# Optimization experiments

Hardware: AMD Instinct MI355X
Metric: run time of the kernel (lower is better)

The kernel has to match this reference:

```python
import jax, jax.numpy as jnp
import numpy as np

B, H, L, D = 1, 8, 2048, 64
DP = 3   # positional coord dim
RE = 1   # extra relative features appended via concat
F = DP + RE  # LazyLinear in-features


def setup_inputs() -> dict:
    key = jax.random.key(0)
    ks = jax.random.split(key, 12)
    return {
        "q": jax.random.normal(ks[0], (B, H, L, D), jnp.float32),
        "k": jax.random.normal(ks[1], (B, H, L, D), jnp.float32),
        "v": jax.random.normal(ks[2], (B, H, L, D), jnp.float32),
        "c": jax.random.uniform(ks[3], (B, 1, 1, L), jnp.float32),
        "d_q": jax.random.normal(ks[4], (B, L, DP), jnp.float32),
        "d_k_top": jax.random.normal(ks[5], (B, L, DP), jnp.float32),
        "d_k_bot": jax.random.normal(ks[6], (B, L, DP), jnp.float32),
        "d_k_score": jax.random.uniform(ks[7], (B, L, 2, F), jnp.float32),
        "relative_top": jax.random.normal(ks[8], (B, L, L, RE), jnp.float32),
        "relative_bottom": jax.random.normal(ks[9], (B, L, L, RE), jnp.float32),
        "W_w": jax.random.normal(ks[10], (F, H), jnp.float32) * 0.1,
        "W_b": jax.random.normal(ks[11], (F, H), jnp.float32) * 0.1,
    }


def _pairwise_diff(a, b):
    # a: [B,Lq,Dp], b: [B,Lk,Dp] -> [B,Lq,Lk,Dp]
    return a[:, :, None, :] - b[:, None, :, :]


def reference(q, k, v, c, d_q, d_k_top, d_k_bot, d_k_score,
              relative_top, relative_bottom, W_w, W_b):
    # score function: scaled dot product -> [B,H,Lq,Lk]
    scores = jnp.einsum('bhqd,bhkd->bhqk', q, k) * (q.shape[-1] ** -0.5)

    # relative-position bias path
    dt = jnp.concatenate([_pairwise_diff(d_q, d_k_top), relative_top], axis=-1)     # [B,Lq,Lk,F]
    db = jnp.concatenate([_pairwise_diff(d_q, d_k_bot), relative_bottom], axis=-1)  # [B,Lq,Lk,F]
    dm = jnp.stack([dt, db], axis=3)                 # [B,Lq,Lk,2,F]
    dm = dm * d_k_score[:, None]                     # broadcast over Lq
    dm = dm.sum(axis=3)                              # [B,Lq,Lk,F]

    w = jax.nn.softplus(dm @ W_w).transpose(0, 3, 1, 2)  # [B,H,Lq,Lk]
    b = (dm @ W_b).transpose(0, 3, 1, 2)                 # [B,H,Lq,Lk]
    scores = scores * w + b

    # leaky probability function: softmax gated by per-key sampling weights c
    probs = jax.nn.softmax(scores, axis=-1) * c      # [B,H,Lq,Lk]

    out = jnp.einsum('bhqk,bhkd->bhqd', probs, v)
    return out, probs
```

## Files before the change

### kernel.cpp

```cpp
#include <hip/hip_runtime.h>
#include <cstdint>
#include <cstddef>

#define NH 8
#define LQ 2048
#define DH 64
#define NKT_HALF 16

typedef __attribute__((ext_vector_type(8))) __bf16 bf16x8;
typedef __attribute__((ext_vector_type(8))) unsigned short ushort8;
typedef __attribute__((ext_vector_type(4))) float floatx4;

__device__ __forceinline__ unsigned short bf_trunc(float x) {
    return (unsigned short)(__float_as_uint(x) >> 16);
}
__device__ __forceinline__ float bf_up(unsigned short h) {
    return __uint_as_float(((unsigned int)h) << 16);
}
__device__ __forceinline__ unsigned short bf_rne(float x) {
    unsigned int u = __float_as_uint(x);
    return (unsigned short)((u + 0x7FFFu + ((u >> 16) & 1u)) >> 16);
}
struct hl_t { unsigned short h, l; };
__device__ __forceinline__ hl_t split2(float x) {
    hl_t r;
    r.h = bf_trunc(x);
    r.l = bf_trunc(x - bf_up(r.h));
    return r;
}

#define MFMA16(A, B, C) __builtin_amdgcn_mfma_f32_16x16x32_bf16((A), (B), (C), 0, 0, 0)

__global__ __launch_bounds__(256, 3) void attn_main(
    const float* __restrict__ qp,  const float* __restrict__ kp,
    const float* __restrict__ vp,  const float* __restrict__ cp,
    const float* __restrict__ dqp, const float* __restrict__ dktp,
    const float* __restrict__ dkbp,const float* __restrict__ dksp,
    const float* __restrict__ rtp, const float* __restrict__ rbp,
    const float* __restrict__ Wwp, const float* __restrict__ Wbp,
    float* __restrict__ probp, float* __restrict__ lws, float* __restrict__ pvws)
{
    __shared__ unsigned short sh_khi[64 * 72];
    __shared__ unsigned short sh_klo[64 * 72];
    __shared__ unsigned short sh_vhi[64 * 72];
    __shared__ unsigned short sh_vlo[64 * 72];
    __shared__ float sh_meta[64 * 13];
    __shared__ float sh_dqs[64 * 3];

    const int bid  = blockIdx.x;
    const int half = bid & 1;
    const int h    = (bid >> 1) & 7;
    const int qt   = bid >> 4;
    const int q0   = qt * 64;
    const int t    = threadIdx.x;
    const int lane = t & 63;
    const int m    = lane & 15;
    const int quad = lane >> 4;
    const int w16  = (t >> 6) * 16;

    float Ww[4], Wb[4];
#pragma unroll
    for (int f = 0; f < 4; ++f) { Ww[f] = Wwp[f * NH + h]; Wb[f] = Wbp[f * NH + h]; }

    {
        const int row = t >> 2, s = t & 3;
        const float* src = qp + ((size_t)(h * LQ + q0 + row)) * DH + s * 16;
        ushort8 vh0, vh1, vl0, vl1;
#pragma unroll
        for (int j = 0; j < 2; ++j) {
            float4 x = *(const float4*)(src + 4 * j);
            hl_t a = split2(x.x), b = split2(x.y), c = split2(x.z), d = split2(x.w);
            vh0[4 * j + 0] = a.h; vl0[4 * j + 0] = a.l;
            vh0[4 * j + 1] = b.h; vl0[4 * j + 1] = b.l;
            vh0[4 * j + 2] = c.h; vl0[4 * j + 2] = c.l;
            vh0[4 * j + 3] = d.h; vl0[4 * j + 3] = d.l;
        }
#pragma unroll
        for (int j = 0; j < 2; ++j) {
            float4 x = *(const float4*)(src + 8 + 4 * j);
            hl_t a = split2(x.x), b = split2(x.y), c = split2(x.z), d = split2(x.w);
            vh1[4 * j + 0] = a.h; vl1[4 * j + 0] = a.l;
            vh1[4 * j + 1] = b.h; vl1[4 * j + 1] = b.l;
            vh1[4 * j + 2] = c.h; vl1[4 * j + 2] = c.l;
            vh1[4 * j + 3] = d.h; vl1[4 * j + 3] = d.l;
        }
        const int base = row * 72 + s * 16;
        *(ushort8*)&sh_khi[base] = vh0;  *(ushort8*)&sh_khi[base + 8] = vh1;
        *(ushort8*)&sh_klo[base] = vl0;  *(ushort8*)&sh_klo[base + 8] = vl1;
        if (t < 64) {
            sh_dqs[t * 3 + 0] = dqp[(q0 + t) * 3 + 0];
            sh_dqs[t * 3 + 1] = dqp[(q0 + t) * 3 + 1];
            sh_dqs[t * 3 + 2] = dqp[(q0 + t) * 3 + 2];
        }
    }
    __syncthreads();

    bf16x8 aqh[2], aql[2];
#pragma unroll
    for (int kc = 0; kc < 2; ++kc) {
        aqh[kc] = *(const bf16x8*)&sh_khi[(w16 + m) * 72 + kc * 32 + quad * 8];
        aql[kc] = *(const bf16x8*)&sh_klo[(w16 + m) * 72 + kc * 32 + quad * 8];
    }
    float dq0[4], dq1[4], dq2[4];
#pragma unroll
    for (int r = 0; r < 4; ++r) {
        const int row = w16 + quad * 4 + r;
        dq0[r] = sh_dqs[row * 3 + 0]; dq1[r] = sh_dqs[row * 3 + 1]; dq2[r] = sh_dqs[row * 3 + 2];
    }
    __syncthreads();

    const floatx4 zf = {0.f, 0.f, 0.f, 0.f};
    floatx4 pacc[4] = {zf, zf, zf, zf};
    float lpart[4] = {0.f, 0.f, 0.f, 0.f};

    for (int kth = 0; kth < NKT_HALF; ++kth) {
        const int k0 = (half * NKT_HALF + kth) * 64;

        {
            const int row = t >> 2, s = t & 3;
            const float* src = kp + ((size_t)(h * LQ + k0 + row)) * DH + s * 16;
            ushort8 vh0, vh1, vl0, vl1;
#pragma unroll
            for (int j = 0; j < 2; ++j) {
                float4 x = *(const float4*)(src + 4 * j);
                hl_t a = split2(x.x), b = split2(x.y), c = split2(x.z), d = split2(x.w);
                vh0[4 * j + 0] = a.h; vl0[4 * j + 0] = a.l;
                vh0[4 * j + 1] = b.h; vl0[4 * j + 1] = b.l;
                vh0[4 * j + 2] = c.h; vl0[4 * j + 2] = c.l;
                vh0[4 * j + 3] = d.h; vl0[4 * j + 3] = d.l;
            }
#pragma unroll
            for (int j = 0; j < 2; ++j) {
                float4 x = *(const float4*)(src + 8 + 4 * j);
                hl_t a = split2(x.x), b = split2(x.y), c = split2(x.z), d = split2(x.w);
                vh1[4 * j + 0] = a.h; vl1[4 * j + 0] = a.l;
                vh1[4 * j + 1] = b.h; vl1[4 * j + 1] = b.l;
                vh1[4 * j + 2] = c.h; vl1[4 * j + 2] = c.l;
                vh1[4 * j + 3] = d.h; vl1[4 * j + 3] = d.l;
            }
            const int base = row * 72 + s * 16;
            *(ushort8*)&sh_khi[base] = vh0;  *(ushort8*)&sh_khi[base + 8] = vh1;
            *(ushort8*)&sh_klo[base] = vl0;  *(ushort8*)&sh_klo[base + 8] = vl1;
        }
        {
            const int p = t >> 4;
            const int mm = t & 15;
#pragma unroll
            for (int g = 0; g < 2; ++g) {
                const int kka = 2 * p + 32 * g;
                const float ca = cp[k0 + kka], cb = cp[k0 + kka + 1];
                const float* va = vp + ((size_t)(h * LQ + k0 + kka)) * DH;
                const float* vb = va + DH;
#pragma unroll
                for (int dd = 0; dd < 4; ++dd) {
                    const int d = mm + 16 * dd;
                    hl_t xa = split2(va[d] * ca);
                    hl_t xb = split2(vb[d] * cb);
                    *(unsigned int*)&sh_vhi[d * 72 + kka] = (unsigned int)xa.h | ((unsigned int)xb.h << 16);
                    *(unsigned int*)&sh_vlo[d * 72 + kka] = (unsigned int)xa.l | ((unsigned int)xb.l << 16);
                }
            }
        }
        if (t < 64) {
            const int kg = k0 + t;
            const float* sc_ = dksp + (size_t)kg * 8;
            const float* tp  = dktp + (size_t)kg * 3;
            const float* bt  = dkbp + (size_t)kg * 3;
            float cw = 0.f, cb2 = 0.f;
#pragma unroll
            for (int f = 0; f < 3; ++f) {
                const float stf = sc_[f], sbf = sc_[4 + f];
                const float A  = stf + sbf;
                const float Bv = tp[f] * stf + bt[f] * sbf;
                sh_meta[t * 13 + f]     = A * Ww[f];
                sh_meta[t * 13 + 4 + f] = A * Wb[f];
                cw  -= Bv * Ww[f];
                cb2 -= Bv * Wb[f];
            }
            sh_meta[t * 13 + 3]  = cw;              sh_meta[t * 13 + 7]  = cb2;
            sh_meta[t * 13 + 8]  = sc_[3] * Ww[3];  sh_meta[t * 13 + 9]  = sc_[7] * Ww[3];
            sh_meta[t * 13 + 10] = sc_[3] * Wb[3];  sh_meta[t * 13 + 11] = sc_[7] * Wb[3];
        }
        __syncthreads();

        float rt_[4][4], rb_[4][4];
#pragma unroll
        for (int r = 0; r < 4; ++r) {
            const size_t q = (size_t)(q0 + w16 + quad * 4 + r);
#pragma unroll
            for (int nt = 0; nt < 4; ++nt) {
                rt_[nt][r] = rtp[q * LQ + k0 + nt * 16 + m];
                rb_[nt][r] = rbp[q * LQ + k0 + nt * 16 + m];
            }
        }

        floatx4 sc[4] = {zf, zf, zf, zf};
#pragma unroll
        for (int nt = 0; nt < 4; ++nt) {
#pragma unroll
            for (int kc = 0; kc < 2; ++kc) {
                const int kb = (nt * 16 + m) * 72 + kc * 32 + quad * 8;
                bf16x8 bh = *(const bf16x8*)&sh_khi[kb];
                bf16x8 bl = *(const bf16x8*)&sh_klo[kb];
                sc[nt] = MFMA16(aqh[kc], bh, sc[nt]);
                sc[nt] = MFMA16(aql[kc], bh, sc[nt]);
                sc[nt] = MFMA16(aqh[kc], bl, sc[nt]);
            }
        }
        __syncthreads();

        unsigned short* ebf = sh_klo;
#pragma unroll
        for (int nt = 0; nt < 4; ++nt) {
            const int kcol = nt * 16 + m;
            const float m0 = sh_meta[kcol * 13 + 0],  m1 = sh_meta[kcol * 13 + 1];
            const float m2 = sh_meta[kcol * 13 + 2],  m3 = sh_meta[kcol * 13 + 3];
            const float m4 = sh_meta[kcol * 13 + 4],  m5 = sh_meta[kcol * 13 + 5];
            const float m6 = sh_meta[kcol * 13 + 6],  m7 = sh_meta[kcol * 13 + 7];
            const float m8 = sh_meta[kcol * 13 + 8],  m9 = sh_meta[kcol * 13 + 9];
            const float mA = sh_meta[kcol * 13 + 10], mB = sh_meta[kcol * 13 + 11];
#pragma unroll
            for (int r = 0; r < 4; ++r) {
                float ww = fmaf(dq0[r], m0, m3); ww = fmaf(dq1[r], m1, ww); ww = fmaf(dq2[r], m2, ww);
                ww = fmaf(rt_[nt][r], m8, ww);   ww = fmaf(rb_[nt][r], m9, ww);
                float bb = fmaf(dq0[r], m4, m7); bb = fmaf(dq1[r], m5, bb); bb = fmaf(dq2[r], m6, bb);
                bb = fmaf(rt_[nt][r], mA, bb);   bb = fmaf(rb_[nt][r], mB, bb);
                const float wg = fmaxf(ww, 0.f) + __logf(1.f + __expf(-fabsf(ww)));
                const float sv = fmaf(sc[nt][r] * 0.125f, wg, bb);
                const float e  = __expf(sv - 8.0f);
                lpart[r] += e;
                probp[((size_t)(h * LQ + q0 + w16 + quad * 4 + r)) * LQ + k0 + kcol] = e;
                ebf[(w16 + quad * 4 + r) * 72 + kcol] = bf_rne(e);
            }
        }

        bf16x8 ap0 = *(const bf16x8*)&ebf[(w16 + m) * 72 + quad * 8];
        bf16x8 ap1 = *(const bf16x8*)&ebf[(w16 + m) * 72 + 32 + quad * 8];
#pragma unroll
        for (int nt = 0; nt < 4; ++nt) {
            const int vb = (nt * 16 + m) * 72 + quad * 8;
            bf16x8 bh0 = *(const bf16x8*)&sh_vhi[vb];
            bf16x8 bl0 = *(const bf16x8*)&sh_vlo[vb];
            bf16x8 bh1 = *(const bf16x8*)&sh_vhi[vb + 32];
            bf16x8 bl1 = *(const bf16x8*)&sh_vlo[vb + 32];
            pacc[nt] = MFMA16(ap0, bh0, pacc[nt]);
            pacc[nt] = MFMA16(ap0, bl0, pacc[nt]);
            pacc[nt] = MFMA16(ap1, bh1, pacc[nt]);
            pacc[nt] = MFMA16(ap1, bl1, pacc[nt]);
        }
        __syncthreads();
    }

#pragma unroll
    for (int off = 1; off < 16; off <<= 1) {
#pragma unroll
        for (int r = 0; r < 4; ++r) lpart[r] += __shfl_xor(lpart[r], off, 64);
    }
    if (m == 0) {
#pragma unroll
        for (int r = 0; r < 4; ++r)
            lws[half * (NH * LQ) + h * LQ + q0 + w16 + quad * 4 + r] = lpart[r];
    }
#pragma unroll
    for (int nt = 0; nt < 4; ++nt) {
#pragma unroll
        for (int r = 0; r < 4; ++r) {
            const size_t row = (size_t)(h * LQ + q0 + w16 + quad * 4 + r);
            pvws[(size_t)half * (NH * LQ * DH) + row * DH + nt * 16 + m] = pacc[nt][r];
        }
    }
}

__global__ void combine_kernel(const float* __restrict__ pvws, const float* __restrict__ lws,
                               float* __restrict__ outp)
{
    const int idx4 = blockIdx.x * 256 + threadIdx.x;
    const int row  = idx4 >> 4;
    const int d4   = (idx4 & 15) * 4;
    const float4 a = *(const float4*)(pvws + (size_t)row * DH + d4);
    const float4 b = *(const float4*)(pvws + (size_t)(NH * LQ * DH) + (size_t)row * DH + d4);
    const float rl = 1.0f / (lws[row] + lws[NH * LQ + row]);
    *(float4*)(outp + (size_t)row * DH + d4) =
        make_float4((a.x + b.x) * rl, (a.y + b.y) * rl, (a.z + b.z) * rl, (a.w + b.w) * rl);
}

__global__ void norm_kernel(float* __restrict__ probp, const float* __restrict__ cp,
                            const float* __restrict__ lws)
{
    const int row = blockIdx.x;
    const float rl = 1.0f / (lws[row] + lws[NH * LQ + row]);
    float* p = probp + (size_t)row * LQ;
    const int t = threadIdx.x;
    float4 x0 = *(const float4*)(p + t * 4);
    float4 x1 = *(const float4*)(p + (t + 256) * 4);
    const float4 c0 = *(const float4*)(cp + t * 4);
    const float4 c1 = *(const float4*)(cp + (t + 256) * 4);
    x0.x *= rl * c0.x; x0.y *= rl * c0.y; x0.z *= rl * c0.z; x0.w *= rl * c0.w;
    x1.x *= rl * c1.x; x1.y *= rl * c1.y; x1.z *= rl * c1.z; x1.w *= rl * c1.w;
    *(float4*)(p + t * 4)         = x0;
    *(float4*)(p + (t + 256) * 4) = x1;
}

extern "C" void kernel_launch(void* const* d_in, const int* in_sizes, int n_in,
                              void* d_out, int out_size, void* d_ws, size_t ws_size,
                              hipStream_t stream)
{
    (void)in_sizes; (void)n_in; (void)ws_size; (void)out_size;
    const float* qp   = (const float*)d_in[0];
    const float* kp   = (const float*)d_in[1];
    const float* vp   = (const float*)d_in[2];
    const float* cp   = (const float*)d_in[3];
    const float* dqp  = (const float*)d_in[4];
    const float* dktp = (const float*)d_in[5];
    const float* dkbp = (const float*)d_in[6];
    const float* dksp = (const float*)d_in[7];
    const float* rtp  = (const float*)d_in[8];
    const float* rbp  = (const float*)d_in[9];
    const float* Wwp  = (const float*)d_in[10];
    const float* Wbp  = (const float*)d_in[11];

    float* outp  = (float*)d_out;
    float* probp = (float*)d_out + (size_t)NH * LQ * DH;

    float* lws  = (float*)d_ws;
    float* pvws = (float*)d_ws + 2 * (NH * LQ);

    attn_main<<<dim3(512), dim3(256), 0, stream>>>(
        qp, kp, vp, cp, dqp, dktp, dkbp, dksp, rtp, rbp, Wwp, Wbp, probp, lws, pvws);
    combine_kernel<<<dim3(1024), dim3(256), 0, stream>>>(pvws, lws, outp);
    norm_kernel<<<dim3(NH * LQ), dim3(256), 0, stream>>>(probp, cp, lws);
}
```

Measured before the change: 293.7 us.

## Fuse combine and prob-normalization into main kernel via pairwise block handshake

Removes the separate combine and norm kernels. Each pair of blocks, one per key half of a query tile, now signals through an atomic counter and spins until its partner finishes. It then normalizes its half of the probs rows, which are probably still in cache, and the half-0 block combines the two PV partial outputs. This saves two launches and a second full pass over probs from cold memory. The spin-wait could deadlock if a partner block is not co-resident, and a memset of the counters is added before the launch.

```diff
diff --git a/kernel.cpp b/kernel.cpp
--- a/kernel.cpp
+++ b/kernel.cpp
@@ -38,7 +38,8 @@
     const float* __restrict__ dkbp,const float* __restrict__ dksp,
     const float* __restrict__ rtp, const float* __restrict__ rbp,
     const float* __restrict__ Wwp, const float* __restrict__ Wbp,
-    float* __restrict__ probp, float* __restrict__ lws, float* __restrict__ pvws)
+    float* __restrict__ probp, float* __restrict__ lws, float* __restrict__ pvws,
+    unsigned int* __restrict__ cnt, float* __restrict__ outp)
 {
     __shared__ unsigned short sh_khi[64 * 72];
     __shared__ unsigned short sh_klo[64 * 72];
@@ -269,36 +270,49 @@
             pvws[(size_t)half * (NH * LQ * DH) + row * DH + nt * 16 + m] = pacc[nt][r];
         }
     }
-}
-
-__global__ void combine_kernel(const float* __restrict__ pvws, const float* __restrict__ lws,
-                               float* __restrict__ outp)
-{
-    const int idx4 = blockIdx.x * 256 + threadIdx.x;
-    const int row  = idx4 >> 4;
-    const int d4   = (idx4 & 15) * 4;
-    const float4 a = *(const float4*)(pvws + (size_t)row * DH + d4);
-    const float4 b = *(const float4*)(pvws + (size_t)(NH * LQ * DH) + (size_t)row * DH + d4);
-    const float rl = 1.0f / (lws[row] + lws[NH * LQ + row]);
-    *(float4*)(outp + (size_t)row * DH + d4) =
-        make_float4((a.x + b.x) * rl, (a.y + b.y) * rl, (a.z + b.z) * rl, (a.w + b.w) * rl);
-}
-
-__global__ void norm_kernel(float* __restrict__ probp, const float* __restrict__ cp,
-                            const float* __restrict__ lws)
-{
-    const int row = blockIdx.x;
-    const float rl = 1.0f / (lws[row] + lws[NH * LQ + row]);
-    float* p = probp + (size_t)row * LQ;
-    const int t = threadIdx.x;
-    float4 x0 = *(const float4*)(p + t * 4);
-    float4 x1 = *(const float4*)(p + (t + 256) * 4);
-    const float4 c0 = *(const float4*)(cp + t * 4);
-    const float4 c1 = *(const float4*)(cp + (t + 256) * 4);
-    x0.x *= rl * c0.x; x0.y *= rl * c0.y; x0.z *= rl * c0.z; x0.w *= rl * c0.w;
-    x1.x *= rl * c1.x; x1.y *= rl * c1.y; x1.z *= rl * c1.z; x1.w *= rl * c1.w;
-    *(float4*)(p + t * 4)         = x0;
-    *(float4*)(p + (t + 256) * 4) = x1;
+
+    __threadfence();
+    __syncthreads();
+    if (t == 0) {
+        __hip_atomic_fetch_add(&cnt[bid >> 1], 1u, __ATOMIC_RELEASE, __HIP_MEMORY_SCOPE_AGENT);
+        while (__hip_atomic_load(&cnt[bid >> 1], __ATOMIC_ACQUIRE, __HIP_MEMORY_SCOPE_AGENT) < 2u) {
+            __builtin_amdgcn_s_sleep(8);
+        }
+    }
+    __syncthreads();
+    __threadfence();
+
+    if (t < 64) {
+        const int row = h * LQ + q0 + t;
+        sh_dqs[t] = 1.0f / (lws[row] + lws[NH * LQ + row]);
+    }
+    __syncthreads();
+
+    {
+        const float4 c4 = *(const float4*)(cp + half * 1024 + (t << 2));
+        float* pbase = probp + ((size_t)(h * LQ + q0)) * LQ + half * 1024 + (t << 2);
+#pragma unroll 4
+        for (int r = 0; r < 64; ++r) {
+            const float rl = sh_dqs[r];
+            float4 x = *(const float4*)(pbase + (size_t)r * LQ);
+            x.x *= rl * c4.x; x.y *= rl * c4.y; x.z *= rl * c4.z; x.w *= rl * c4.w;
+            *(float4*)(pbase + (size_t)r * LQ) = x;
+        }
+    }
+
+    if (half == 0) {
+        const int r  = t >> 2;
+        const int cs = (t & 3) * 16;
+        const size_t row = (size_t)(h * LQ + q0 + r);
+        const float rl = sh_dqs[r];
+#pragma unroll
+        for (int j = 0; j < 4; ++j) {
+            float4 a = *(const float4*)(pvws + row * DH + cs + 4 * j);
+            float4 b = *(const float4*)(pvws + (size_t)(NH * LQ * DH) + row * DH + cs + 4 * j);
+            *(float4*)(outp + row * DH + cs + 4 * j) =
+                make_float4((a.x + b.x) * rl, (a.y + b.y) * rl, (a.z + b.z) * rl, (a.w + b.w) * rl);
+        }
+    }
 }
 
 extern "C" void kernel_launch(void* const* d_in, const int* in_sizes, int n_in,
@@ -324,9 +338,10 @@
 
     float* lws  = (float*)d_ws;
     float* pvws = (float*)d_ws + 2 * (NH * LQ);
+    unsigned int* cnt = (unsigned int*)(pvws + (size_t)2 * (NH * LQ * DH));
+
+    hipMemsetAsync(cnt, 0, 256 * sizeof(unsigned int), stream);
 
     attn_main<<<dim3(512), dim3(256), 0, stream>>>(
-        qp, kp, vp, cp, dqp, dktp, dkbp, dksp, rtp, rbp, Wwp, Wbp, probp, lws, pvws);
-    combine_kernel<<<dim3(1024), dim3(256), 0, stream>>>(pvws, lws, outp);
-    norm_kernel<<<dim3(NH * LQ), dim3(256), 0, stream>>>(probp, cp, lws);
-}
+        qp, kp, vp, cp, dqp, dktp, dkbp, dksp, rtp, rbp, Wwp, Wbp, probp, lws, pvws, cnt, outp);
+}
```

Result: slower. 475.5 us (+61.9%).

## Precompute split-bf16 K/V and per-key bias metadata in a prep kernel

Applied to the files above, without the earlier changes.

Adds a prep kernel that converts K (pre-scaled by 1/sqrt(D)) and c-scaled V into hi/lo bf16 planes in workspace, storing V pre-transposed per tile, and computes per-key bias metadata once per head. The main kernel then copies these tiles straight into shared memory instead of redoing the conversion and metadata math in every query-tile block. This removes work repeated across the 32 query tiles that share each key tile. The cost is an extra launch plus extra workspace traffic, and it only takes effect when the workspace is large enough, otherwise the old path runs.

```diff
diff --git a/kernel.cpp b/kernel.cpp
--- a/kernel.cpp
+++ b/kernel.cpp
@@ -31,6 +31,93 @@
 
 #define MFMA16(A, B, C) __builtin_amdgcn_mfma_f32_16x16x32_bf16((A), (B), (C), 0, 0, 0)
 
+__global__ __launch_bounds__(256) void prep_kernel(
+    const float* __restrict__ kp,  const float* __restrict__ vp,
+    const float* __restrict__ cp,  const float* __restrict__ dktp,
+    const float* __restrict__ dkbp,const float* __restrict__ dksp,
+    const float* __restrict__ Wwp, const float* __restrict__ Wbp,
+    unsigned short* __restrict__ khig, unsigned short* __restrict__ klog,
+    unsigned short* __restrict__ vhig, unsigned short* __restrict__ vlog,
+    float* __restrict__ metag)
+{
+    const int bid = blockIdx.x;
+    const int t   = threadIdx.x;
+
+    if (bid < 256) {
+        const int h = bid >> 5, kt = bid & 31;
+        const int row = t >> 2, s = t & 3;
+        const size_t kg = (size_t)(h * LQ) + kt * 64 + row;
+        const float* src = kp + kg * DH + s * 16;
+        unsigned short* dh_ = khig + kg * DH + s * 16;
+        unsigned short* dl_ = klog + kg * DH + s * 16;
+        ushort8 vh0, vh1, vl0, vl1;
+#pragma unroll
+        for (int j = 0; j < 2; ++j) {
+            float4 x = *(const float4*)(src + 4 * j);
+            hl_t a = split2(x.x * 0.125f), b = split2(x.y * 0.125f);
+            hl_t c = split2(x.z * 0.125f), d = split2(x.w * 0.125f);
+            vh0[4*j+0]=a.h; vl0[4*j+0]=a.l; vh0[4*j+1]=b.h; vl0[4*j+1]=b.l;
+            vh0[4*j+2]=c.h; vl0[4*j+2]=c.l; vh0[4*j+3]=d.h; vl0[4*j+3]=d.l;
+        }
+#pragma unroll
+        for (int j = 0; j < 2; ++j) {
+            float4 x = *(const float4*)(src + 8 + 4 * j);
+            hl_t a = split2(x.x * 0.125f), b = split2(x.y * 0.125f);
+            hl_t c = split2(x.z * 0.125f), d = split2(x.w * 0.125f);
+            vh1[4*j+0]=a.h; vl1[4*j+0]=a.l; vh1[4*j+1]=b.h; vl1[4*j+1]=b.l;
+            vh1[4*j+2]=c.h; vl1[4*j+2]=c.l; vh1[4*j+3]=d.h; vl1[4*j+3]=d.l;
+        }
+        *(ushort8*)&dh_[0] = vh0; *(ushort8*)&dh_[8] = vh1;
+        *(ushort8*)&dl_[0] = vl0; *(ushort8*)&dl_[8] = vl1;
+    } else if (bid < 512) {
+        const int h = (bid - 256) >> 5, kt = (bid - 256) & 31;
+        const int p = t >> 4, mm = t & 15;
+        const int k0 = kt * 64;
+#pragma unroll
+        for (int g = 0; g < 2; ++g) {
+            const int kka = 2 * p + 32 * g;
+            const float ca = cp[k0 + kka], cb = cp[k0 + kka + 1];
+            const float* va = vp + ((size_t)(h * LQ + k0 + kka)) * DH;
+            const float* vb = va + DH;
+#pragma unroll
+            for (int dd = 0; dd < 4; ++dd) {
+                const int d = mm + 16 * dd;
+                hl_t xa = split2(va[d] * ca);
+                hl_t xb = split2(vb[d] * cb);
+                const size_t base = ((size_t)(h * 32 + kt) * 64 + d) * 64 + kka;
+                *(unsigned int*)&vhig[base] = (unsigned int)xa.h | ((unsigned int)xb.h << 16);
+                *(unsigned int*)&vlog[base] = (unsigned int)xa.l | ((unsigned int)xb.l << 16);
+            }
+        }
+    } else {
+        const int idx = (bid - 512) * 256 + t;
+        const int h  = idx >> 11;
+        const int kg = idx & 2047;
+        float Ww[4], Wb[4];
+#pragma unroll
+        for (int f = 0; f < 4; ++f) { Ww[f] = Wwp[f * NH + h]; Wb[f] = Wbp[f * NH + h]; }
+        const float* sc_ = dksp + (size_t)kg * 8;
+        const float* tp  = dktp + (size_t)kg * 3;
+        const float* bt  = dkbp + (size_t)kg * 3;
+        float* mo = metag + ((size_t)(h * LQ) + kg) * 12;
+        float cw = 0.f, cb2 = 0.f;
+#pragma unroll
+        for (int f = 0; f < 3; ++f) {
+            const float stf = sc_[f], sbf = sc_[4 + f];
+            const float A  = stf + sbf;
+            const float Bv = tp[f] * stf + bt[f] * sbf;
+            mo[f]     = A * Ww[f];
+            mo[4 + f] = A * Wb[f];
+            cw  -= Bv * Ww[f];
+            cb2 -= Bv * Wb[f];
+        }
+        mo[3]  = cw;              mo[7]  = cb2;
+        mo[8]  = sc_[3] * Ww[3];  mo[9]  = sc_[7] * Ww[3];
+        mo[10] = sc_[3] * Wb[3];  mo[11] = sc_[7] * Wb[3];
+    }
+}
+
+template<int PRE>
 __global__ __launch_bounds__(256, 3) void attn_main(
     const float* __restrict__ qp,  const float* __restrict__ kp,
     const float* __restrict__ vp,  const float* __restrict__ cp,
@@ -38,13 +125,16 @@
     const float* __restrict__ dkbp,const float* __restrict__ dksp,
     const float* __restrict__ rtp, const float* __restrict__ rbp,
     const float* __restrict__ Wwp, const float* __restrict__ Wbp,
+    const unsigned short* __restrict__ khig, const unsigned short* __restrict__ klog,
+    const unsigned short* __restrict__ vhig, const unsigned short* __restrict__ vlog,
+    const float* __restrict__ metag,
     float* __restrict__ probp, float* __restrict__ lws, float* __restrict__ pvws)
 {
     __shared__ unsigned short sh_khi[64 * 72];
     __shared__ unsigned short sh_klo[64 * 72];
     __shared__ unsigned short sh_vhi[64 * 72];
     __shared__ unsigned short sh_vlo[64 * 72];
-    __shared__ float sh_meta[64 * 13];
+    __shared__ float sh_meta[64 * 12];
     __shared__ float sh_dqs[64 * 3];
 
     const int bid  = blockIdx.x;
@@ -59,8 +149,10 @@
     const int w16  = (t >> 6) * 16;
 
     float Ww[4], Wb[4];
-#pragma unroll
-    for (int f = 0; f < 4; ++f) { Ww[f] = Wwp[f * NH + h]; Wb[f] = Wbp[f * NH + h]; }
+    if constexpr (!PRE) {
+#pragma unroll
+        for (int f = 0; f < 4; ++f) { Ww[f] = Wwp[f * NH + h]; Wb[f] = Wbp[f * NH + h]; }
+    }
 
     {
         const int row = t >> 2, s = t & 3;
@@ -70,19 +162,15 @@
         for (int j = 0; j < 2; ++j) {
             float4 x = *(const float4*)(src + 4 * j);
             hl_t a = split2(x.x), b = split2(x.y), c = split2(x.z), d = split2(x.w);
-            vh0[4 * j + 0] = a.h; vl0[4 * j + 0] = a.l;
-            vh0[4 * j + 1] = b.h; vl0[4 * j + 1] = b.l;
-            vh0[4 * j + 2] = c.h; vl0[4 * j + 2] = c.l;
-            vh0[4 * j + 3] = d.h; vl0[4 * j + 3] = d.l;
+            vh0[4*j+0]=a.h; vl0[4*j+0]=a.l; vh0[4*j+1]=b.h; vl0[4*j+1]=b.l;
+            vh0[4*j+2]=c.h; vl0[4*j+2]=c.l; vh0[4*j+3]=d.h; vl0[4*j+3]=d.l;
         }
 #pragma unroll
         for (int j = 0; j < 2; ++j) {
             float4 x = *(const float4*)(src + 8 + 4 * j);
             hl_t a = split2(x.x), b = split2(x.y), c = split2(x.z), d = split2(x.w);
-            vh1[4 * j + 0] = a.h; vl1[4 * j + 0] = a.l;
-            vh1[4 * j + 1] = b.h; vl1[4 * j + 1] = b.l;
-            vh1[4 * j + 2] = c.h; vl1[4 * j + 2] = c.l;
-            vh1[4 * j + 3] = d.h; vl1[4 * j + 3] = d.l;
+            vh1[4*j+0]=a.h; vl1[4*j+0]=a.l; vh1[4*j+1]=b.h; vl1[4*j+1]=b.l;
+            vh1[4*j+2]=c.h; vl1[4*j+2]=c.l; vh1[4*j+3]=d.h; vl1[4*j+3]=d.l;
         }
         const int base = row * 72 + s * 16;
         *(ushort8*)&sh_khi[base] = vh0;  *(ushort8*)&sh_khi[base + 8] = vh1;
@@ -116,70 +204,92 @@
     for (int kth = 0; kth < NKT_HALF; ++kth) {
         const int k0 = (half * NKT_HALF + kth) * 64;
 
-        {
-            const int row = t >> 2, s = t & 3;
-            const float* src = kp + ((size_t)(h * LQ + k0 + row)) * DH + s * 16;
-            ushort8 vh0, vh1, vl0, vl1;
-#pragma unroll
-            for (int j = 0; j < 2; ++j) {
-                float4 x = *(const float4*)(src + 4 * j);
-                hl_t a = split2(x.x), b = split2(x.y), c = split2(x.z), d = split2(x.w);
-                vh0[4 * j + 0] = a.h; vl0[4 * j + 0] = a.l;
-                vh0[4 * j + 1] = b.h; vl0[4 * j + 1] = b.l;
-                vh0[4 * j + 2] = c.h; vl0[4 * j + 2] = c.l;
-                vh0[4 * j + 3] = d.h; vl0[4 * j + 3] = d.l;
-            }
-#pragma unroll
-            for (int j = 0; j < 2; ++j) {
-                float4 x = *(const float4*)(src + 8 + 4 * j);
-                hl_t a = split2(x.x), b = split2(x.y), c = split2(x.z), d = split2(x.w);
-                vh1[4 * j + 0] = a.h; vl1[4 * j + 0] = a.l;
-                vh1[4 * j + 1] = b.h; vl1[4 * j + 1] = b.l;
-                vh1[4 * j + 2] = c.h; vl1[4 * j + 2] = c.l;
-                vh1[4 * j + 3] = d.h; vl1[4 * j + 3] = d.l;
-            }
-            const int base = row * 72 + s * 16;
-            *(ushort8*)&sh_khi[base] = vh0;  *(ushort8*)&sh_khi[base + 8] = vh1;
-            *(ushort8*)&sh_klo[base] = vl0;  *(ushort8*)&sh_klo[base + 8] = vl1;
-        }
-        {
-            const int p = t >> 4;
-            const int mm = t & 15;
-#pragma unroll
-            for (int g = 0; g < 2; ++g) {
-                const int kka = 2 * p + 32 * g;
-                const float ca = cp[k0 + kka], cb = cp[k0 + kka + 1];
-                const float* va = vp + ((size_t)(h * LQ + k0 + kka)) * DH;
-                const float* vb = va + DH;
-#pragma unroll
-                for (int dd = 0; dd < 4; ++dd) {
-                    const int d = mm + 16 * dd;
-                    hl_t xa = split2(va[d] * ca);
-                    hl_t xb = split2(vb[d] * cb);
-                    *(unsigned int*)&sh_vhi[d * 72 + kka] = (unsigned int)xa.h | ((unsigned int)xb.h << 16);
-                    *(unsigned int*)&sh_vlo[d * 72 + kka] = (unsigned int)xa.l | ((unsigned int)xb.l << 16);
+        if constexpr (PRE) {
+            {
+                const int row = t >> 2, s = t & 3;
+                const size_t gb = ((size_t)(h * LQ) + k0 + row) * DH + s * 16;
+                const int base = row * 72 + s * 16;
+                *(ushort8*)&sh_khi[base]     = *(const ushort8*)&khig[gb];
+                *(ushort8*)&sh_khi[base + 8] = *(const ushort8*)&khig[gb + 8];
+                *(ushort8*)&sh_klo[base]     = *(const ushort8*)&klog[gb];
+                *(ushort8*)&sh_klo[base + 8] = *(const ushort8*)&klog[gb + 8];
+            }
+            {
+                const int row = t >> 2, s = t & 3;
+                const size_t gb = ((size_t)(h * 32 + (k0 >> 6)) * 64 + row) * 64 + s * 16;
+                const int base = row * 72 + s * 16;
+                *(ushort8*)&sh_vhi[base]     = *(const ushort8*)&vhig[gb];
+                *(ushort8*)&sh_vhi[base + 8] = *(const ushort8*)&vhig[gb + 8];
+                *(ushort8*)&sh_vlo[base]     = *(const ushort8*)&vlog[gb];
+                *(ushort8*)&sh_vlo[base + 8] = *(const ushort8*)&vlog[gb + 8];
+            }
+            if (t < 192) {
+                const int k = t / 3, j = t - k * 3;
+                const float4 mv = *(const float4*)(metag + ((size_t)(h * LQ) + k0 + k) * 12 + j * 4);
+                *(float4*)&sh_meta[k * 12 + j * 4] = mv;
+            }
+        } else {
+            {
+                const int row = t >> 2, s = t & 3;
+                const float* src = kp + ((size_t)(h * LQ + k0 + row)) * DH + s * 16;
+                ushort8 vh0, vh1, vl0, vl1;
+#pragma unroll
+                for (int j = 0; j < 2; ++j) {
+                    float4 x = *(const float4*)(src + 4 * j);
+                    hl_t a = split2(x.x), b = split2(x.y), c = split2(x.z), d = split2(x.w);
+                    vh0[4*j+0]=a.h; vl0[4*j+0]=a.l; vh0[4*j+1]=b.h; vl0[4*j+1]=b.l;
+                    vh0[4*j+2]=c.h; vl0[4*j+2]=c.l; vh0[4*j+3]=d.h; vl0[4*j+3]=d.l;
                 }
-            }
-        }
-        if (t < 64) {
-            const int kg = k0 + t;
-            const float* sc_ = dksp + (size_t)kg * 8;
-            const float* tp  = dktp + (size_t)kg * 3;
-            const float* bt  = dkbp + (size_t)kg * 3;
-            float cw = 0.f, cb2 = 0.f;
-#pragma unroll
-            for (int f = 0; f < 3; ++f) {
-                const float stf = sc_[f], sbf = sc_[4 + f];
-                const float A  = stf + sbf;
-                const float Bv = tp[f] * stf + bt[f] * sbf;
-                sh_meta[t * 13 + f]     = A * Ww[f];
-                sh_meta[t * 13 + 4 + f] = A * Wb[f];
-                cw  -= Bv * Ww[f];
-                cb2 -= Bv * Wb[f];
-            }
-            sh_meta[t * 13 + 3]  = cw;              sh_meta[t * 13 + 7]  = cb2;
-            sh_meta[t * 13 + 8]  = sc_[3] * Ww[3];  sh_meta[t * 13 + 9]  = sc_[7] * Ww[3];
-            sh_meta[t * 13 + 10] = sc_[3] * Wb[3];  sh_meta[t * 13 + 11] = sc_[7] * Wb[3];
+#pragma unroll
+                for (int j = 0; j < 2; ++j) {
+                    float4 x = *(const float4*)(src + 8 + 4 * j);
+                    hl_t a = split2(x.x), b = split2(x.y), c = split2(x.z), d = split2(x.w);
+                    vh1[4*j+0]=a.h; vl1[4*j+0]=a.l; vh1[4*j+1]=b.h; vl1[4*j+1]=b.l;
+                    vh1[4*j+2]=c.h; vl1[4*j+2]=c.l; vh1[4*j+3]=d.h; vl1[4*j+3]=d.l;
+                }
+                const int base = row * 72 + s * 16;
+                *(ushort8*)&sh_khi[base] = vh0;  *(ushort8*)&sh_khi[base + 8] = vh1;
+                *(ushort8*)&sh_klo[base] = vl0;  *(ushort8*)&sh_klo[base + 8] = vl1;
+            }
+            {
+                const int p = t >> 4;
+                const int mm = t & 15;
+#pragma unroll
+                for (int g = 0; g < 2; ++g) {
+                    const int kka = 2 * p + 32 * g;
+                    const float ca = cp[k0 + kka], cb = cp[k0 + kka + 1];
+                    const float* va = vp + ((size_t)(h * LQ + k0 + kka)) * DH;
+                    const float* vb = va + DH;
+#pragma unroll
+                    for (int dd = 0; dd < 4; ++dd) {
+                        const int d = mm + 16 * dd;
+                        hl_t xa = split2(va[d] * ca);
+                        hl_t xb = split2(vb[d] * cb);
+                        *(unsigned int*)&sh_vhi[d * 72 + kka] = (unsigned int)xa.h | ((unsigned int)xb.h << 16);
+                        *(unsigned int*)&sh_vlo[d * 72 + kka] = (unsigned int)xa.l | ((unsigned int)xb.l << 16);
+                    }
+                }
+            }
+            if (t < 64) {
+                const int kg = k0 + t;
+                const float* sc_ = dksp + (size_t)kg * 8;
+                const float* tp  = dktp + (size_t)kg * 3;
+                const float* bt  = dkbp + (size_t)kg * 3;
+                float cw = 0.f, cb2 = 0.f;
+#pragma unroll
+                for (int f = 0; f < 3; ++f) {
+                    const float stf = sc_[f], sbf = sc_[4 + f];
+                    const float A  = stf + sbf;
+                    const float Bv = tp[f] * stf + bt[f] * sbf;
+                    sh_meta[t * 12 + f]     = A * Ww[f];
+                    sh_meta[t * 12 + 4 + f] = A * Wb[f];
+                    cw  -= Bv * Ww[f];
+                    cb2 -= Bv * Wb[f];
+                }
+                sh_meta[t * 12 + 3]  = cw;              sh_meta[t * 12 + 7]  = cb2;
+                sh_meta[t * 12 + 8]  = sc_[3] * Ww[3];  sh_meta[t * 12 + 9]  = sc_[7] * Ww[3];
+                sh_meta[t * 12 + 10] = sc_[3] * Wb[3];  sh_meta[t * 12 + 11] = sc_[7] * Wb[3];
+            }
         }
         __syncthreads();
 
@@ -213,12 +323,12 @@
 #pragma unroll
         for (int nt = 0; nt < 4; ++nt) {
             const int kcol = nt * 16 + m;
-            const float m0 = sh_meta[kcol * 13 + 0],  m1 = sh_meta[kcol * 13 + 1];
-            const float m2 = sh_meta[kcol * 13 + 2],  m3 = sh_meta[kcol * 13 + 3];
-            const float m4 = sh_meta[kcol * 13 + 4],  m5 = sh_meta[kcol * 13 + 5];
-            const float m6 = sh_meta[kcol * 13 + 6],  m7 = sh_meta[kcol * 13 + 7];
-            const float m8 = sh_meta[kcol * 13 + 8],  m9 = sh_meta[kcol * 13 + 9];
-            const float mA = sh_meta[kcol * 13 + 10], mB = sh_meta[kcol * 13 + 11];
+            const float m0 = sh_meta[kcol * 12 + 0],  m1 = sh_meta[kcol * 12 + 1];
+            const float m2 = sh_meta[kcol * 12 + 2],  m3 = sh_meta[kcol * 12 + 3];
+            const float m4 = sh_meta[kcol * 12 + 4],  m5 = sh_meta[kcol * 12 + 5];
+            const float m6 = sh_meta[kcol * 12 + 6],  m7 = sh_meta[kcol * 12 + 7];
+            const float m8 = sh_meta[kcol * 12 + 8],  m9 = sh_meta[kcol * 12 + 9];
+            const float mA = sh_meta[kcol * 12 + 10], mB = sh_meta[kcol * 12 + 11];
 #pragma unroll
             for (int r = 0; r < 4; ++r) {
                 float ww = fmaf(dq0[r], m0, m3); ww = fmaf(dq1[r], m1, ww); ww = fmaf(dq2[r], m2, ww);
@@ -226,7 +336,9 @@
                 float bb = fmaf(dq0[r], m4, m7); bb = fmaf(dq1[r], m5, bb); bb = fmaf(dq2[r], m6, bb);
                 bb = fmaf(rt_[nt][r], mA, bb);   bb = fmaf(rb_[nt][r], mB, bb);
                 const float wg = fmaxf(ww, 0.f) + __logf(1.f + __expf(-fabsf(ww)));
-                const float sv = fmaf(sc[nt][r] * 0.125f, wg, bb);
+                float sv;
+                if constexpr (PRE) sv = fmaf(sc[nt][r], wg, bb);
+                else               sv = fmaf(sc[nt][r] * 0.125f, wg, bb);
                 const float e  = __expf(sv - 8.0f);
                 lpart[r] += e;
                 probp[((size_t)(h * LQ + q0 + w16 + quad * 4 + r)) * LQ + k0 + kcol] = e;
@@ -305,7 +417,7 @@
                               void* d_out, int out_size, void* d_ws, size_t ws_size,
                               hipStream_t stream)
 {
-    (void)in_sizes; (void)n_in; (void)ws_size; (void)out_size;
+    (void)in_sizes; (void)n_in; (void)out_size;
     const float* qp   = (const float*)d_in[0];
     const float* kp   = (const float*)d_in[1];
     const float* vp   = (const float*)d_in[2];
@@ -323,10 +435,29 @@
     float* probp = (float*)d_out + (size_t)NH * LQ * DH;
 
     float* lws  = (float*)d_ws;
-    float* pvws = (float*)d_ws + 2 * (NH * LQ);
-
-    attn_main<<<dim3(512), dim3(256), 0, stream>>>(
-        qp, kp, vp, cp, dqp, dktp, dkbp, dksp, rtp, rbp, Wwp, Wbp, probp, lws, pvws);
+    float* pvws = lws + 2 * (NH * LQ);
+    unsigned short* khig = (unsigned short*)(pvws + (size_t)2 * NH * LQ * DH);
+    unsigned short* klog = khig + (size_t)NH * LQ * DH;
+    unsigned short* vhig = klog + (size_t)NH * LQ * DH;
+    unsigned short* vlog = vhig + (size_t)NH * LQ * DH;
+    float* metag = (float*)(vlog + (size_t)NH * LQ * DH);
+
+    const size_t need = (size_t)2 * NH * LQ * 4
+                      + (size_t)2 * NH * LQ * DH * 4
+                      + (size_t)4 * NH * LQ * DH * 2
+                      + (size_t)NH * LQ * 12 * 4;
+
+    if (ws_size >= need) {
+        prep_kernel<<<dim3(576), dim3(256), 0, stream>>>(
+            kp, vp, cp, dktp, dkbp, dksp, Wwp, Wbp, khig, klog, vhig, vlog, metag);
+        attn_main<1><<<dim3(512), dim3(256), 0, stream>>>(
+            qp, kp, vp, cp, dqp, dktp, dkbp, dksp, rtp, rbp, Wwp, Wbp,
+            khig, klog, vhig, vlog, metag, probp, lws, pvws);
+    } else {
+        attn_main<0><<<dim3(512), dim3(256), 0, stream>>>(
+            qp, kp, vp, cp, dqp, dktp, dkbp, dksp, rtp, rbp, Wwp, Wbp,
+            nullptr, nullptr, nullptr, nullptr, nullptr, probp, lws, pvws);
+    }
     combine_kernel<<<dim3(1024), dim3(256), 0, stream>>>(pvws, lws, outp);
     norm_kernel<<<dim3(NH * LQ), dim3(256), 0, stream>>>(probp, cp, lws);
 }
```

New measurement: 287.3 us. 2.2% less time.
